# Kernel optimization log

Hardware: AMD Instinct MI355X
Metric: run time of the kernel (lower is better)

## Reference

```python
import jax, jax.numpy as jnp
import numpy as np

D = 256
NH = 8
HD = D // NH
B, HH, WW = 4, 28, 28
EPS = 1e-5

def _ln(x, g, b):
    m = jnp.mean(x, -1, keepdims=True)
    v = jnp.var(x, -1, keepdims=True)
    return (x - m) * jax.lax.rsqrt(v + EPS) * g + b

def _heads(x):
    b, n, _ = x.shape
    return x.reshape(b, n, NH, HD)

def _attn(q, k, v):
    # q,k,v: [B,N,D] -> multi-head SDPA, full NxN scores as in source
    qh, kh, vh = _heads(q), _heads(k), _heads(v)
    s = jnp.einsum('bqhd,bkhd->bhqk', qh, kh) * (HD ** -0.5)
    a = jax.nn.softmax(s, axis=-1)
    o = jnp.einsum('bhqk,bkhd->bqhd', a, vh)
    return o.reshape(q.shape)

def setup_inputs():
    key = jax.random.key(0)
    ks = iter(jax.random.split(key, 80))
    def rn(shape, s):
        return jax.random.normal(next(ks), shape, jnp.float32) * s
    w = D ** -0.5
    inp = {}
    for n in ('f1', 'f2', 'f3', 'f4'):
        inp[n] = rn((B, D, HH, WW), 1.0)
    for n in ('Wq_a', 'Wk_a', 'Wv_a', 'Wq_b', 'Wk_b', 'Wv_b'):
        inp[n] = rn((4, D, D), w)
    for n in ('bq_a', 'bk_a', 'bv_a', 'bq_b', 'bk_b', 'bv_b'):
        inp[n] = jnp.zeros((4, D), jnp.float32)
    inp['gamma'] = rn((4,), 0.5)
    inp['gamma_ffn'] = rn((4,), 0.5)
    inp['Wfuse'] = rn((4, 2 * D, D), w)
    inp['bfuse'] = jnp.zeros((4, D), jnp.float32)
    inp['W1'] = rn((4, D, 4 * D), w)
    inp['b1'] = jnp.zeros((4, 4 * D), jnp.float32)
    inp['W2'] = rn((4, 4 * D, D), (4 * D) ** -0.5)
    inp['b2'] = jnp.zeros((4, D), jnp.float32)
    inp['ln1_g'] = jnp.ones((4, D), jnp.float32)
    inp['ln1_b'] = jnp.zeros((4, D), jnp.float32)
    inp['ln2_g'] = jnp.ones((4, D), jnp.float32)
    inp['ln2_b'] = jnp.zeros((4, D), jnp.float32)
    inp['fp_ln_g'] = jnp.ones((D,), jnp.float32)
    inp['fp_ln_b'] = jnp.zeros((D,), jnp.float32)
    inp['fp_W'] = rn((D, D), w)
    inp['fp_b'] = jnp.zeros((D,), jnp.float32)
    inp['ff_ln_g'] = jnp.ones((4 * D,), jnp.float32)
    inp['ff_ln_b'] = jnp.zeros((4 * D,), jnp.float32)
    inp['ff_W'] = rn((4 * D, D), (4 * D) ** -0.5)
    inp['ff_b'] = jnp.zeros((D,), jnp.float32)
    inp['mha_Wqkv'] = rn((D, 3 * D), w)
    inp['mha_bqkv'] = jnp.zeros((3 * D,), jnp.float32)
    inp['mha_Wo'] = rn((D, D), w)
    inp['mha_bo'] = jnp.zeros((D,), jnp.float32)
    inp['norm_g'] = jnp.ones((D,), jnp.float32)
    inp['norm_b'] = jnp.zeros((D,), jnp.float32)
    return inp

def reference(f1, f2, f3, f4, Wq_a, Wk_a, Wv_a, Wq_b, Wk_b, Wv_b,
              bq_a, bk_a, bv_a, bq_b, bk_b, bv_b, gamma, gamma_ffn,
              Wfuse, bfuse, W1, b1, W2, b2, ln1_g, ln1_b, ln2_g, ln2_b,
              fp_ln_g, fp_ln_b, fp_W, fp_b, ff_ln_g, ff_ln_b, ff_W, ff_b,
              mha_Wqkv, mha_bqkv, mha_Wo, mha_bo, norm_g, norm_b):
    to_seq = lambda x: x.transpose(0, 2, 3, 1).reshape(x.shape[0], -1, x.shape[1])

    def block(i, xa, xb):
        # BiDirectionalCrossAttention.forward (dropout inactive in eval)
        qa = xa @ Wq_a[i] + bq_a[i]
        kb = xb @ Wk_b[i] + bk_b[i]
        vb = xb @ Wv_b[i] + bv_b[i]
        qb = xb @ Wq_b[i] + bq_b[i]
        ka = xa @ Wk_a[i] + bk_a[i]
        va = xa @ Wv_a[i] + bv_a[i]
        a2b = _attn(qa, kb, vb)
        b2a = _attn(qb, ka, va)
        fused = jnp.concatenate([a2b, b2a], -1) @ Wfuse[i] + bfuse[i]
        xa1 = _ln(xa + jnp.tanh(gamma[i]) * fused, ln1_g[i], ln1_b[i])
        ffn = jax.nn.gelu(xa1 @ W1[i] + b1[i], approximate=False) @ W2[i] + b2[i]
        return _ln(xa1 + jnp.tanh(gamma_ffn[i]) * ffn, ln2_g[i], ln2_b[i])

    s1, s2, s3, s4 = to_seq(f1), to_seq(f2), to_seq(f3), to_seq(f4)
    # block indices: 0=cross_attn_1_2, 1=cross_attn_1_4, 2=cross_attn_2_3, 3=cross_attn_3_4
    e1 = (block(0, s1, s2) + block(1, s1, s4)) / 2
    e2 = (block(0, s2, s1) + block(2, s2, s3)) / 2
    e3 = (block(2, s3, s2) + block(3, s3, s4)) / 2
    e4 = (block(1, s4, s1) + block(3, s4, s3)) / 2
    fp = lambda x: jax.nn.gelu(_ln(x, fp_ln_g, fp_ln_b) @ fp_W + fp_b, approximate=False)
    allf = jnp.concatenate([fp(e1), fp(e2), fp(e3), fp(e4)], -1)
    x = jax.nn.gelu(_ln(allf, ff_ln_g, ff_ln_b) @ ff_W + ff_b, approximate=False)
    # nn.MultiheadAttention self-attention (no residual in source)
    qkv = x @ mha_Wqkv + mha_bqkv
    q, k, v = jnp.split(qkv, 3, axis=-1)
    attn_out = _attn(q, k, v) @ mha_Wo + mha_bo
    x = _ln(attn_out, norm_g, norm_b)
    return x.reshape(B, HH, WW, D).transpose(0, 3, 1, 2)
```

## Files before the change

### kernel.cpp

```cpp
#include <hip/hip_runtime.h>

typedef unsigned short u16;
typedef __bf16 bf16x8 __attribute__((ext_vector_type(8)));
typedef float f32x4 __attribute__((ext_vector_type(4)));
typedef float f32x16 __attribute__((ext_vector_type(16)));
typedef unsigned short u16x8 __attribute__((ext_vector_type(8)));
typedef unsigned short u16x4 __attribute__((ext_vector_type(4)));

static constexpr size_t MD = 802816;

__device__ __forceinline__ u16 f2bf(float f) {
    __bf16 h = (__bf16)f;
    return __builtin_bit_cast(unsigned short, h);
}
__device__ __forceinline__ float bf2f(u16 u) {
    return __uint_as_float(((unsigned)u) << 16);
}
__device__ __forceinline__ float gelu_f(float x) {
    return 0.5f * x * (1.0f + erff(x * 0.70710678118654752f));
}
__device__ __forceinline__ unsigned cvt_pk_bf16(float a, float b) {
    unsigned r;
    asm("v_cvt_pk_bf16_f32 %0, %1, %2" : "=v"(r) : "v"(a), "v"(b));
    return r;
}
__device__ __forceinline__ float exp2_hw(float x) {
    float r;
    asm("v_exp_f32 %0, %1" : "=v"(r) : "v"(x));
    return r;
}
__device__ __forceinline__ int xcd_swz(int id, int nwg) {
    int q = nwg >> 3, r = nwg & 7;
    int xcd = id & 7, idx = id >> 3;
    return (xcd < r) ? (xcd * (q + 1) + idx) : (r * (q + 1) + (xcd - r) * q + idx);
}
union u8_4 { u16x8 v8; u16x4 v4[2]; };
union bf8_4 { bf16x8 f; u16x4 h[2]; u16x8 v8; };

__device__ __forceinline__ void gemm_core(
    const u16* __restrict__ A, int lda,
    const u16* __restrict__ Bt, int K,
    const float* __restrict__ bias,
    u16* __restrict__ C, int ldc, int act, int m0, int n0,
    u16* __restrict__ VT)
{
    __shared__ u16 As[64][72];
    __shared__ u16 Bs[64][72];
    const int tid  = threadIdx.x;
    const int wave = tid >> 6, lane = tid & 63;
    const int wr = wave >> 1, wc = wave & 1;
    const int l16 = lane & 15, kg = lane >> 4, kb = kg * 8;
    const int srow = tid >> 2, scol = (tid & 3) * 16;

    f32x4 acc[2][2];
#pragma unroll
    for (int j = 0; j < 2; j++)
#pragma unroll
        for (int i = 0; i < 2; i++) { f32x4 z = {0.f,0.f,0.f,0.f}; acc[j][i] = z; }

    const u16* ap = A + (size_t)(m0 + srow) * lda + scol;
    const u16* bp = Bt + (size_t)(n0 + srow) * K + scol;
    u16x8 ua0 = *(const u16x8*)ap;
    u16x8 ua1 = *(const u16x8*)(ap + 8);
    u16x8 ub0 = *(const u16x8*)bp;
    u16x8 ub1 = *(const u16x8*)(bp + 8);

    for (int kt = 0; kt < K; kt += 64) {
        *(u16x8*)&As[srow][scol]     = ua0;
        *(u16x8*)&As[srow][scol + 8] = ua1;
        *(u16x8*)&Bs[srow][scol]     = ub0;
        *(u16x8*)&Bs[srow][scol + 8] = ub1;
        __syncthreads();
        if (kt + 64 < K) {
            ua0 = *(const u16x8*)(ap + kt + 64);
            ua1 = *(const u16x8*)(ap + kt + 72);
            ub0 = *(const u16x8*)(bp + kt + 64);
            ub1 = *(const u16x8*)(bp + kt + 72);
        }
#pragma unroll
        for (int h = 0; h < 2; h++) {
            bf16x8 af[2], bf[2];
#pragma unroll
            for (int j = 0; j < 2; j++)
                af[j] = *(const bf16x8*)&Bs[wc*32 + j*16 + l16][h*32 + kb];
#pragma unroll
            for (int i = 0; i < 2; i++)
                bf[i] = *(const bf16x8*)&As[wr*32 + i*16 + l16][h*32 + kb];
#pragma unroll
            for (int j = 0; j < 2; j++)
#pragma unroll
                for (int i = 0; i < 2; i++)
                    acc[j][i] = __builtin_amdgcn_mfma_f32_16x16x32_bf16(
                        af[j], bf[i], acc[j][i], 0,0,0);
        }
        __syncthreads();
    }
#pragma unroll
    for (int j = 0; j < 2; j++) {
        int lcol = wc*32 + j*16 + kg*4;
        f32x4 bv = *(const f32x4*)&bias[n0 + lcol];
#pragma unroll
        for (int i = 0; i < 2; i++) {
            int lrow = wr*32 + i*16 + l16;
            u16x4 o;
#pragma unroll
            for (int r = 0; r < 4; r++) {
                float v = acc[j][i][r] + bv[r];
                if (act == 1) v = gelu_f(v);
                o[r] = f2bf(v);
            }
            *(u16x4*)&As[lrow][lcol] = o;
        }
    }
    __syncthreads();
    if (VT && n0 >= 512) {
        int c = tid & 63, chunk = tid >> 6;
        int dg = n0 - 512 + c;
        int hh2 = dg >> 5, dd = dg & 31;
        int grow = m0 + chunk*16;
        int bb2 = grow / 784, kk0 = grow - bb2 * 784;
        u16x8 a, b;
#pragma unroll
        for (int j = 0; j < 8; j++) a[j] = As[chunk*16 + j][c];
#pragma unroll
        for (int j = 0; j < 8; j++) b[j] = As[chunk*16 + 8 + j][c];
        u16* vp = VT + ((size_t)(bb2*8 + hh2)*32 + dd)*784 + kk0;
        *(u16x8*)vp = a;
        *(u16x8*)(vp + 8) = b;
    } else {
        int crow = tid >> 2, cc = (tid & 3) * 16;
        u16x8 c0 = *(const u16x8*)&As[crow][cc];
        u16x8 c1 = *(const u16x8*)&As[crow][cc + 8];
        u16* cp = &C[(size_t)(m0 + crow) * ldc + n0 + cc];
        *(u16x8*)cp = c0;
        *(u16x8*)(cp + 8) = c1;
    }
}

__global__ __launch_bounds__(256) void gemm2_kernel(
    const u16* __restrict__ A, int lda, int zA,
    const u16* __restrict__ Bt, int K, int i0, int i1, int i2, int i3, int Bsz,
    const float* __restrict__ bias, int bN,
    u16* __restrict__ C, int ldc, int zC, int act, int nN, int nwg)
{
    int wg = xcd_swz(blockIdx.x, nwg);
    int n = wg % nN, rest = wg / nN;
    int m = rest % 49, z = rest / 49;
    int iz = (z == 0) ? i0 : (z == 1) ? i1 : (z == 2) ? i2 : i3;
    gemm_core(A + (size_t)z * zA, lda,
              Bt + (size_t)iz * Bsz, K,
              bias + (size_t)iz * bN,
              C + (size_t)z * zC, ldc, act, m * 64, n * 64, nullptr);
}

__global__ __launch_bounds__(256) void proj8_kernel(
    const u16* __restrict__ s, int b0, int b1, int b2, int b3,
    int i0, int i1, int i2, int i3,
    const u16* __restrict__ projWt, const float* __restrict__ biasc,
    u16* __restrict__ projc, u16* __restrict__ vt)
{
    int wg = xcd_swz(blockIdx.x, 4704);
    int n = wg % 12, rest = wg / 12;
    int m = rest % 49, z = rest / 49;
    int inv = z >> 1, ab = z & 1;
    int bi = (inv == 0) ? b0 : (inv == 1) ? b1 : (inv == 2) ? b2 : b3;
    int ii = (inv == 0) ? i0 : (inv == 1) ? i1 : (inv == 2) ? i2 : i3;
    const u16* Aact = s + (size_t)(ab ? bi : inv) * MD;
    int widx = ii * 2 + ab;
    gemm_core(Aact, 256, projWt + (size_t)widx * 768 * 256, 256,
              biasc + widx * 768,
              projc + (size_t)z * 3 * MD, 768, 0, m * 64, n * 64,
              vt + (size_t)(z ^ 1) * MD);
}

__global__ __launch_bounds__(256) void pack_bias_kernel(
    const float* b0, const float* b1, const float* b2,
    const float* b3, const float* b4, const float* b5,
    float* __restrict__ biasc)
{
    int z = blockIdx.x;
    int tsr = z >> 2, i = z & 3;
    const float* barr[6] = {b0,b1,b2,b3,b4,b5};
    int ab = (tsr >= 3) ? 1 : 0;
    biasc[(i*2 + ab)*768 + (tsr % 3)*256 + threadIdx.x] = barr[tsr][i*256 + threadIdx.x];
}

__device__ __forceinline__ void attn3_core(
    const u16* __restrict__ Qg, int ldq,
    const u16* __restrict__ Kg, int ldk,
    const u16* __restrict__ Vtg,
    u16* __restrict__ Og, int ldo,
    int qt, int rowbase, int qkcol, int ocol)
{
    __shared__ u16 Ks[2][64][36];
    __shared__ u16 Vts[2][32][68];
    __shared__ u16 Ps[4][32][68];
    __shared__ float Ls[4][32];

    const int tid = threadIdx.x, wave = tid >> 6, lane = tid & 63;
    const int l32 = lane & 31, hi = lane >> 5;
    const int sr = tid >> 2, sc8 = (tid & 3) * 8;
    const int vd = tid >> 3, vk8 = (tid & 7) * 8;
    const float QSC = 0.25503489f;

    bf8_4 qf0, qf1;
    {
        int qrow = qt*128 + wave*32 + l32;
        u16x8 z8 = {0,0,0,0,0,0,0,0};
        u16x8 q0 = z8, q1 = z8;
        if (qrow < 784) {
            const u16* qp = Qg + (size_t)(rowbase + qrow) * ldq + qkcol;
            q0 = *(const u16x8*)(qp + hi*8);
            q1 = *(const u16x8*)(qp + 16 + hi*8);
        }
#pragma unroll
        for (int j = 0; j < 8; j++) {
            q0[j] = f2bf(bf2f(q0[j]) * QSC);
            q1[j] = f2bf(bf2f(q1[j]) * QSC);
        }
        qf0.v8 = q0;
        qf1.v8 = q1;
    }
    {
        u8_4 k, v;
        k.v8 = *(const u16x8*)(Kg + (size_t)(rowbase + sr) * ldk + qkcol + sc8);
        v.v8 = *(const u16x8*)(Vtg + (size_t)vd * 784 + vk8);
        *(u16x4*)&Ks[0][sr][sc8]     = k.v4[0];
        *(u16x4*)&Ks[0][sr][sc8 + 4] = k.v4[1];
        *(u16x4*)&Vts[0][vd][vk8]     = v.v4[0];
        *(u16x4*)&Vts[0][vd][vk8 + 4] = v.v4[1];
    }
    __syncthreads();

    f32x16 oacc;
#pragma unroll
    for (int i = 0; i < 16; i++) oacc[i] = 0.f;
    float lsum = 0.f;

    u16x8 kr, vr;
    for (int t = 0; t < 13; ++t) {
        const int cur = t & 1;
        if (t < 12) {
            u16x8 z8 = {0,0,0,0,0,0,0,0}; kr = z8; vr = z8;
            int krow = (t+1)*64 + sr;
            if (krow < 784)
                kr = *(const u16x8*)(Kg + (size_t)(rowbase + krow) * ldk + qkcol + sc8);
            int kc = (t+1)*64 + vk8;
            if (kc + 7 < 784)
                vr = *(const u16x8*)(Vtg + (size_t)vd * 784 + kc);
        }
        const int kvalid = (t == 12) ? 16 : 64;
#pragma unroll
        for (int kb2 = 0; kb2 < 2; kb2++) {
            f32x16 sacc;
#pragma unroll
            for (int i = 0; i < 16; i++) sacc[i] = 0.f;
            bf8_4 kf0, kf1;
            kf0.h[0] = *(const u16x4*)&Ks[cur][kb2*32 + l32][hi*8];
            kf0.h[1] = *(const u16x4*)&Ks[cur][kb2*32 + l32][hi*8 + 4];
            kf1.h[0] = *(const u16x4*)&Ks[cur][kb2*32 + l32][16 + hi*8];
            kf1.h[1] = *(const u16x4*)&Ks[cur][kb2*32 + l32][16 + hi*8 + 4];
            sacc = __builtin_amdgcn_mfma_f32_32x32x16_bf16(kf0.f, qf0.f, sacc, 0,0,0);
            sacc = __builtin_amdgcn_mfma_f32_32x32x16_bf16(kf1.f, qf1.f, sacc, 0,0,0);
#pragma unroll
            for (int g = 0; g < 4; g++) {
                int k0 = kb2*32 + 8*g + 4*hi;
                union { unsigned u[2]; u16x4 v; } pk;
                if (k0 < kvalid) {
                    float p0 = exp2_hw(sacc[4*g+0]);
                    float p1 = exp2_hw(sacc[4*g+1]);
                    float p2 = exp2_hw(sacc[4*g+2]);
                    float p3 = exp2_hw(sacc[4*g+3]);
                    lsum += (p0 + p1) + (p2 + p3);
                    pk.u[0] = cvt_pk_bf16(p0, p1);
                    pk.u[1] = cvt_pk_bf16(p2, p3);
                } else { pk.u[0] = 0; pk.u[1] = 0; }
                *(u16x4*)&Ps[wave][l32][k0] = pk.v;
            }
        }
#pragma unroll
        for (int kf2 = 0; kf2 < 4; kf2++) {
            bf8_4 pf, vf;
            pf.h[0] = *(const u16x4*)&Ps[wave][l32][kf2*16 + hi*8];
            pf.h[1] = *(const u16x4*)&Ps[wave][l32][kf2*16 + hi*8 + 4];
            vf.h[0] = *(const u16x4*)&Vts[cur][l32][kf2*16 + hi*8];
            vf.h[1] = *(const u16x4*)&Vts[cur][l32][kf2*16 + hi*8 + 4];
            oacc = __builtin_amdgcn_mfma_f32_32x32x16_bf16(pf.f, vf.f, oacc, 0,0,0);
        }
        if (t < 12) {
            u8_4 k, v; k.v8 = kr; v.v8 = vr;
            *(u16x4*)&Ks[cur^1][sr][sc8]     = k.v4[0];
            *(u16x4*)&Ks[cur^1][sr][sc8 + 4] = k.v4[1];
            *(u16x4*)&Vts[cur^1][vd][vk8]     = v.v4[0];
            *(u16x4*)&Vts[cur^1][vd][vk8 + 4] = v.v4[1];
            __syncthreads();
        }
    }
    float lt = lsum + __shfl_xor(lsum, 32);
    if (hi == 0) Ls[wave][l32] = lt;
    f32x4 lv[4];
#pragma unroll
    for (int g = 0; g < 4; g++) lv[g] = *(const f32x4*)&Ls[wave][8*g + 4*hi];
#pragma unroll
    for (int g = 0; g < 4; g++)
#pragma unroll
        for (int j = 0; j < 4; j++) {
            int row = qt*128 + wave*32 + 8*g + 4*hi + j;
            if (row < 784)
                Og[(size_t)(rowbase + row) * ldo + ocol + l32] =
                    f2bf(oacc[4*g+j] * __builtin_amdgcn_rcpf(lv[g][j]));
        }
}

__global__ __launch_bounds__(256) void attn_pair_kernel(
    const u16* __restrict__ projc, const u16* __restrict__ vt,
    u16* __restrict__ fusedin)
{
    int id = blockIdx.x;
    int wg = (id & 7) * 224 + (id >> 3);
    int qt = wg % 7, bh = (wg / 7) & 31, z = wg / 224;
    int inv = z >> 1, dir = z & 1;
    const u16* Q  = projc + (size_t)z * 3 * MD;
    const u16* K  = projc + (size_t)(z ^ 1) * 3 * MD + 256;
    const u16* Vt = vt + (size_t)z * MD + (size_t)bh * 32 * 784;
    u16* O = fusedin + (size_t)inv * 2 * MD;
    int bb = bh >> 3, hh = bh & 7;
    attn3_core(Q, 768, K, 768, Vt, O, 512, qt, bb*784, hh*32, dir*256 + hh*32);
}

__global__ __launch_bounds__(256) void attn_mha_kernel(
    const u16* __restrict__ qkv, const u16* __restrict__ vtmha,
    u16* __restrict__ outp)
{
    int id = blockIdx.x;
    int wg = (id & 7) * 28 + (id >> 3);
    int qt = wg % 7, bh = wg / 7;
    int bb = bh >> 3, hh = bh & 7;
    const u16* Vt = vtmha + (size_t)bh * 32 * 784;
    attn3_core(qkv, 768, qkv + 256, 768, Vt, outp, 256, qt, bb*784, hh*32, hh*32);
}

__global__ __launch_bounds__(256) void ln_kernel(
    const u16* __restrict__ x, int zx,
    const u16* __restrict__ res, int zres,
    const float* __restrict__ gamma, int i0, int i1, int i2, int i3,
    const float* __restrict__ g, const float* __restrict__ beta, int gN,
    u16* __restrict__ out, int zout,
    float outscale, int accum, int D)
{
    int z = blockIdx.y;
    int iz = (z == 0) ? i0 : (z == 1) ? i1 : (z == 2) ? i2 : i3;
    const u16* xb = x + (size_t)z * zx;
    const u16* rb = res ? res + (size_t)z * zres : (const u16*)nullptr;
    u16* ob = out + (size_t)z * zout;
    const float* gg = g + iz * gN;
    const float* bb = beta + iz * gN;
    int wave = threadIdx.x >> 6, lane = threadIdx.x & 63;
    int half = lane >> 5, l32 = lane & 31;
    size_t row = (size_t)blockIdx.x * 8 + wave * 2 + half;
    float tg = gamma ? tanhf(gamma[iz]) : 1.0f;
    const u16* xr = xb + row * D;
    const u16* rr = rb ? rb + row * D : (const u16*)nullptr;
    float vals[32];
    int nch = D >> 8;
    float s = 0.f, s2 = 0.f;
    for (int c = 0; c < nch; c++) {
        int col = c * 256 + l32 * 8;
        u16x8 v = *(const u16x8*)(xr + col);
        u16x8 r8 = {0,0,0,0,0,0,0,0};
        if (rr) r8 = *(const u16x8*)(rr + col);
#pragma unroll
        for (int j = 0; j < 8; j++) {
            float a = tg * bf2f(v[j]) + bf2f(r8[j]);
            vals[c*8 + j] = a;
            s += a; s2 += a * a;
        }
    }
#pragma unroll
    for (int off = 1; off < 32; off <<= 1) {
        s  += __shfl_xor(s, off);
        s2 += __shfl_xor(s2, off);
    }
    float inv = 1.0f / D;
    float mean = s * inv;
    float var = s2 * inv - mean * mean;
    float rstd = rsqrtf(var + 1e-5f);
    for (int c = 0; c < nch; c++) {
        int col = c * 256 + l32 * 8;
        u16x8 prev = {0,0,0,0,0,0,0,0};
        if (accum) prev = *(const u16x8*)(ob + row*D + col);
        u16x8 o8;
#pragma unroll
        for (int j = 0; j < 8; j++) {
            float o = (vals[c*8 + j] - mean) * rstd * gg[col + j] + bb[col + j];
            o *= outscale;
            if (accum) o += bf2f(prev[j]);
            o8[j] = f2bf(o);
        }
        *(u16x8*)(ob + row*D + col) = o8;
    }
}

__device__ __forceinline__ void transpose_body(const float* in, u16* out, int K, int N)
{
    __shared__ float t[32][33];
    int tx = threadIdx.x, ty = threadIdx.y;
#pragma unroll
    for (int j = 0; j < 4; j++)
        t[ty + j*8][tx] = in[(size_t)(blockIdx.y*32 + ty + j*8) * N + blockIdx.x*32 + tx];
    __syncthreads();
#pragma unroll
    for (int j = 0; j < 4; j++)
        out[(size_t)(blockIdx.x*32 + ty + j*8) * K + blockIdx.y*32 + tx] =
            f2bf(t[tx][ty + j*8]);
}

__global__ __launch_bounds__(256) void transpose_w(const float* __restrict__ in,
                                                   u16* __restrict__ out, int K, int N)
{
    int z = blockIdx.z;
    transpose_body(in + (size_t)z * K * N, out + (size_t)z * K * N, K, N);
}

__global__ __launch_bounds__(256) void transpose_w6(
    const float* w0, const float* w1, const float* w2,
    const float* w3, const float* w4, const float* w5,
    u16* __restrict__ out)
{
    int z = blockIdx.z;
    int tsr = z >> 2, i = z & 3;
    const float* ws[6] = {w0,w1,w2,w3,w4,w5};
    int ab = (tsr >= 3) ? 1 : 0;
    u16* ob = out + (size_t)((i*2 + ab)*3 + (tsr % 3)) * 65536;
    transpose_body(ws[tsr] + (size_t)i * 65536, ob, 256, 256);
}

__global__ __launch_bounds__(256) void vtrans_kernel(
    const u16* __restrict__ base,
    u16* __restrict__ out)
{
    __shared__ u16 t[64][44];
    const u16* in = base + 512;
    int kt = blockIdx.x, bh = blockIdx.y;
    int bb = bh >> 3, hh = bh & 7;
    int tid = threadIdx.x;
    {
        int r = tid >> 2, c8 = (tid & 3) * 8;
        int krow = kt*64 + r;
        u16x8 u = {0,0,0,0,0,0,0,0};
        if (krow < 784)
            u = *(const u16x8*)(in + (size_t)(bb*784 + krow) * 768 + hh*32 + c8);
        *(u16x8*)&t[r][c8] = u;
    }
    __syncthreads();
    int d = tid >> 3, k8 = (tid & 7) * 8;
    if (kt*64 + k8 + 7 < 784) {
        u16x8 u;
#pragma unroll
        for (int j = 0; j < 8; j++) u[j] = t[k8 + j][d];
        *(u16x8*)&out[(size_t)(bh*32 + d) * 784 + kt*64 + k8] = u;
    }
}

__global__ __launch_bounds__(256) void to_seq_kernel(
    const float* f0, const float* f1, const float* f2, const float* f3,
    u16* __restrict__ sbase)
{
    __shared__ float t[16][17];
    int z = blockIdx.z;
    int fi = z & 3, b = z >> 2;
    const float* fs[4] = {f0,f1,f2,f3};
    const float* f = fs[fi] + (size_t)b * 256 * 784;
    u16* s = sbase + (size_t)fi * MD + (size_t)b * 784 * 256;
    int tx = threadIdx.x, ty = threadIdx.y;
    t[ty][tx] = f[(size_t)(blockIdx.y*16 + ty) * 784 + blockIdx.x*16 + tx];
    __syncthreads();
    s[(size_t)(blockIdx.x*16 + ty) * 256 + blockIdx.y*16 + tx] = f2bf(t[tx][ty]);
}

__global__ __launch_bounds__(256) void from_seq_kernel(const u16* __restrict__ y,
                                                       float* __restrict__ out)
{
    __shared__ float t[16][17];
    int b = blockIdx.z;
    const u16* yb = y + (size_t)b * 784 * 256;
    float* ob = out + (size_t)b * 256 * 784;
    int tx = threadIdx.x, ty = threadIdx.y;
    t[ty][tx] = bf2f(yb[(size_t)(blockIdx.x*16 + ty) * 256 + blockIdx.y*16 + tx]);
    __syncthreads();
    ob[(size_t)(blockIdx.y*16 + ty) * 784 + blockIdx.x*16 + tx] = t[tx][ty];
}

extern "C" void kernel_launch(void* const* d_in, const int* in_sizes, int n_in,
                              void* d_out, int out_size, void* d_ws, size_t ws_size,
                              hipStream_t stream)
{
    (void)in_sizes; (void)n_in; (void)out_size; (void)ws_size;
    const float* f0 = (const float*)d_in[0];
    const float* f1 = (const float*)d_in[1];
    const float* f2 = (const float*)d_in[2];
    const float* f3 = (const float*)d_in[3];
    const float* Wq_a = (const float*)d_in[4];
    const float* Wk_a = (const float*)d_in[5];
    const float* Wv_a = (const float*)d_in[6];
    const float* Wq_b = (const float*)d_in[7];
    const float* Wk_b = (const float*)d_in[8];
    const float* Wv_b = (const float*)d_in[9];
    const float* bq_a = (const float*)d_in[10];
    const float* bk_a = (const float*)d_in[11];
    const float* bv_a = (const float*)d_in[12];
    const float* bq_b = (const float*)d_in[13];
    const float* bk_b = (const float*)d_in[14];
    const float* bv_b = (const float*)d_in[15];
    const float* gamma = (const float*)d_in[16];
    const float* gamma_ffn = (const float*)d_in[17];
    const float* Wfuse = (const float*)d_in[18];
    const float* bfuse = (const float*)d_in[19];
    const float* W1 = (const float*)d_in[20];
    const float* b1 = (const float*)d_in[21];
    const float* W2 = (const float*)d_in[22];
    const float* b2 = (const float*)d_in[23];
    const float* ln1_g = (const float*)d_in[24];
    const float* ln1_b = (const float*)d_in[25];
    const float* ln2_g = (const float*)d_in[26];
    const float* ln2_b = (const float*)d_in[27];
    const float* fp_ln_g = (const float*)d_in[28];
    const float* fp_ln_b = (const float*)d_in[29];
    const float* fp_W = (const float*)d_in[30];
    const float* fp_b = (const float*)d_in[31];
    const float* ff_ln_g = (const float*)d_in[32];
    const float* ff_ln_b = (const float*)d_in[33];
    const float* ff_W = (const float*)d_in[34];
    const float* ff_b = (const float*)d_in[35];
    const float* mha_Wqkv = (const float*)d_in[36];
    const float* mha_bqkv = (const float*)d_in[37];
    const float* mha_Wo = (const float*)d_in[38];
    const float* mha_bo = (const float*)d_in[39];
    const float* norm_g = (const float*)d_in[40];
    const float* norm_b = (const float*)d_in[41];

    u16* W = (u16*)d_ws;
    u16* projWt = W;
    u16* fuseWt = projWt + 1572864;
    u16* W1t    = fuseWt + 524288;
    u16* W2t    = W1t + 1048576;
    u16* fpWt   = W2t + 1048576;
    u16* ffWt   = fpWt + 65536;
    u16* qkvWt  = ffWt + 262144;
    u16* WoWt   = qkvWt + 196608;
    float* biasc = (float*)(WoWt + 65536);
    u16* act    = (u16*)(biasc + 6144);

    u16* s     = act;
    u16* e     = act + 4*MD;
    u16* projc = act + 8*MD;
    u16* vt    = act + 32*MD;
    u16* fin   = act + 40*MD;
    u16* ffh  = projc;
    u16* fb   = projc + 16*MD;
    u16* xa1  = projc + 20*MD;
    u16* ffb  = vt;

    to_seq_kernel<<<dim3(49,16,16), dim3(16,16), 0, stream>>>(f0,f1,f2,f3, s);
    transpose_w6<<<dim3(8,8,24), dim3(32,8), 0, stream>>>(Wq_a,Wk_a,Wv_a,Wq_b,Wk_b,Wv_b, projWt);
    pack_bias_kernel<<<24, 256, 0, stream>>>(bq_a,bk_a,bv_a,bq_b,bk_b,bv_b, biasc);
    transpose_w<<<dim3(8,16,4), dim3(32,8), 0, stream>>>(Wfuse, fuseWt, 512, 256);
    transpose_w<<<dim3(32,8,4), dim3(32,8), 0, stream>>>(W1, W1t, 256, 1024);
    transpose_w<<<dim3(8,32,4), dim3(32,8), 0, stream>>>(W2, W2t, 1024, 256);
    transpose_w<<<dim3(8,8,1),  dim3(32,8), 0, stream>>>(fp_W, fpWt, 256, 256);
    transpose_w<<<dim3(8,32,1), dim3(32,8), 0, stream>>>(ff_W, ffWt, 1024, 256);
    transpose_w<<<dim3(24,8,1), dim3(32,8), 0, stream>>>(mha_Wqkv, qkvWt, 256, 768);
    transpose_w<<<dim3(8,8,1),  dim3(32,8), 0, stream>>>(mha_Wo, WoWt, 256, 256);

    const int GI[2][4] = {{0,0,2,1},{1,2,3,3}};
    const int GB[2][4] = {{1,0,1,0},{3,2,3,2}};

    for (int g = 0; g < 2; g++) {
        int i0 = GI[g][0], i1 = GI[g][1], i2 = GI[g][2], i3 = GI[g][3];
        proj8_kernel<<<4704, 256, 0, stream>>>(s,
            GB[g][0], GB[g][1], GB[g][2], GB[g][3], i0, i1, i2, i3,
            projWt, biasc, projc, vt);
        attn_pair_kernel<<<1792, 256, 0, stream>>>(projc, vt, fin);
        gemm2_kernel<<<784, 256, 0, stream>>>(fin, 512, (int)(2*MD),
            fuseWt, 512, i0, i1, i2, i3, 131072, bfuse, 256, fb, 256, (int)MD, 0, 4, 784);
        ln_kernel<<<dim3(392,4), 256, 0, stream>>>(fb, (int)MD,
            s, (int)MD, gamma, i0, i1, i2, i3, ln1_g, ln1_b, 256,
            xa1, (int)MD, 1.0f, 0, 256);
        gemm2_kernel<<<3136, 256, 0, stream>>>(xa1, 256, (int)MD,
            W1t, 256, i0, i1, i2, i3, 262144, b1, 1024, ffh, 1024, (int)(4*MD), 1, 16, 3136);
        gemm2_kernel<<<784, 256, 0, stream>>>(ffh, 1024, (int)(4*MD),
            W2t, 1024, i0, i1, i2, i3, 262144, b2, 256, ffb, 256, (int)MD, 0, 4, 784);
        ln_kernel<<<dim3(392,4), 256, 0, stream>>>(ffb, (int)MD,
            xa1, (int)MD, gamma_ffn, i0, i1, i2, i3, ln2_g, ln2_b, 256,
            e, (int)MD, 0.5f, g, 256);
    }

    u16* ln4    = act + 8*MD;
    u16* allf   = act + 12*MD;
    u16* ffln   = act + 16*MD;
    u16* x2     = act + 20*MD;
    u16* qkv    = act + 21*MD;
    u16* vtmha  = act + 24*MD;
    u16* attn_o = act + 25*MD;
    u16* ymid   = act + 26*MD;
    u16* yfin   = act + 27*MD;

    ln_kernel<<<dim3(392,4), 256, 0, stream>>>(e, (int)MD,
        (const u16*)nullptr, 0, (const float*)nullptr, 0,0,0,0,
        fp_ln_g, fp_ln_b, 0, ln4, (int)MD, 1.0f, 0, 256);
    gemm2_kernel<<<784, 256, 0, stream>>>(ln4, 256, (int)MD,
        fpWt, 256, 0,0,0,0, 0, fp_b, 0, allf, 1024, 256, 1, 4, 784);
    ln_kernel<<<dim3(392,1), 256, 0, stream>>>(allf, 0,
        (const u16*)nullptr, 0, (const float*)nullptr, 0,0,0,0,
        ff_ln_g, ff_ln_b, 0, ffln, 0, 1.0f, 0, 1024);
    gemm2_kernel<<<196, 256, 0, stream>>>(ffln, 1024, 0,
        ffWt, 1024, 0,0,0,0, 0, ff_b, 0, x2, 256, 0, 1, 4, 196);
    gemm2_kernel<<<588, 256, 0, stream>>>(x2, 256, 0,
        qkvWt, 256, 0,0,0,0, 0, mha_bqkv, 0, qkv, 768, 0, 0, 12, 588);
    vtrans_kernel<<<dim3(13,32), 256, 0, stream>>>(qkv, vtmha);
    attn_mha_kernel<<<224, 256, 0, stream>>>(qkv, vtmha, attn_o);
    gemm2_kernel<<<196, 256, 0, stream>>>(attn_o, 256, 0,
        WoWt, 256, 0,0,0,0, 0, mha_bo, 0, ymid, 256, 0, 0, 4, 196);
    ln_kernel<<<dim3(392,1), 256, 0, stream>>>(ymid, 0,
        (const u16*)nullptr, 0, (const float*)nullptr, 0,0,0,0,
        norm_g, norm_b, 0, yfin, 0, 1.0f, 0, 256);
    from_seq_kernel<<<dim3(49,16,4), dim3(16,16), 0, stream>>>(yfin, (float*)d_out);
}
```

Baseline: 366.1 us.

## Merge both block groups into single wide launches and batch weight transposes

When the workspace is large enough, the two sequential groups of four cross-attention blocks run as one set of launches over all eight blocks, doubling grid sizes and halving launch count. The Q/K projection buffer drops the unused V columns (stride 512 instead of 768). The seven weight transpose launches are merged into one kernel driven by a descriptor table. The accumulate-in-LN averaging is replaced by writing both block outputs separately and summing them in the next LN via the residual path. This costs more workspace memory and adds a fallback path when the workspace is too small.

```diff
diff --git a/kernel.cpp b/kernel.cpp
--- a/kernel.cpp
+++ b/kernel.cpp
@@ -139,37 +139,37 @@
 
 __global__ __launch_bounds__(256) void gemm2_kernel(
     const u16* __restrict__ A, int lda, int zA,
-    const u16* __restrict__ Bt, int K, int i0, int i1, int i2, int i3, int Bsz,
+    const u16* __restrict__ Bt, int K, int ipack, int Bsz,
     const float* __restrict__ bias, int bN,
     u16* __restrict__ C, int ldc, int zC, int act, int nN, int nwg)
 {
     int wg = xcd_swz(blockIdx.x, nwg);
     int n = wg % nN, rest = wg / nN;
     int m = rest % 49, z = rest / 49;
-    int iz = (z == 0) ? i0 : (z == 1) ? i1 : (z == 2) ? i2 : i3;
+    int iz = (ipack >> (2*z)) & 3;
     gemm_core(A + (size_t)z * zA, lda,
               Bt + (size_t)iz * Bsz, K,
               bias + (size_t)iz * bN,
               C + (size_t)z * zC, ldc, act, m * 64, n * 64, nullptr);
 }
 
-__global__ __launch_bounds__(256) void proj8_kernel(
-    const u16* __restrict__ s, int b0, int b1, int b2, int b3,
-    int i0, int i1, int i2, int i3,
+__global__ __launch_bounds__(256) void proj_kernel(
+    const u16* __restrict__ s, int apack, int bpack, int ipack,
     const u16* __restrict__ projWt, const float* __restrict__ biasc,
-    u16* __restrict__ projc, u16* __restrict__ vt)
-{
-    int wg = xcd_swz(blockIdx.x, 4704);
+    u16* __restrict__ projqk, u16* __restrict__ vt, int nwg)
+{
+    int wg = xcd_swz(blockIdx.x, nwg);
     int n = wg % 12, rest = wg / 12;
     int m = rest % 49, z = rest / 49;
     int inv = z >> 1, ab = z & 1;
-    int bi = (inv == 0) ? b0 : (inv == 1) ? b1 : (inv == 2) ? b2 : b3;
-    int ii = (inv == 0) ? i0 : (inv == 1) ? i1 : (inv == 2) ? i2 : i3;
-    const u16* Aact = s + (size_t)(ab ? bi : inv) * MD;
+    int ai = (apack >> (2*inv)) & 3;
+    int bi = (bpack >> (2*inv)) & 3;
+    int ii = (ipack >> (2*inv)) & 3;
+    const u16* Aact = s + (size_t)(ab ? bi : ai) * MD;
     int widx = ii * 2 + ab;
     gemm_core(Aact, 256, projWt + (size_t)widx * 768 * 256, 256,
               biasc + widx * 768,
-              projc + (size_t)z * 3 * MD, 768, 0, m * 64, n * 64,
+              projqk + (size_t)z * 2 * MD, 512, 0, m * 64, n * 64,
               vt + (size_t)(z ^ 1) * MD);
 }
 
@@ -313,19 +313,20 @@
 }
 
 __global__ __launch_bounds__(256) void attn_pair_kernel(
-    const u16* __restrict__ projc, const u16* __restrict__ vt,
-    u16* __restrict__ fusedin)
+    const u16* __restrict__ projqk, const u16* __restrict__ vt,
+    u16* __restrict__ fin)
 {
     int id = blockIdx.x;
-    int wg = (id & 7) * 224 + (id >> 3);
+    int nper = gridDim.x >> 3;
+    int wg = (id & 7) * nper + (id >> 3);
     int qt = wg % 7, bh = (wg / 7) & 31, z = wg / 224;
     int inv = z >> 1, dir = z & 1;
-    const u16* Q  = projc + (size_t)z * 3 * MD;
-    const u16* K  = projc + (size_t)(z ^ 1) * 3 * MD + 256;
+    const u16* Q  = projqk + (size_t)z * 2 * MD;
+    const u16* K  = projqk + (size_t)(z ^ 1) * 2 * MD + 256;
     const u16* Vt = vt + (size_t)z * MD + (size_t)bh * 32 * 784;
-    u16* O = fusedin + (size_t)inv * 2 * MD;
+    u16* O = fin + (size_t)inv * 2 * MD;
     int bb = bh >> 3, hh = bh & 7;
-    attn3_core(Q, 768, K, 768, Vt, O, 512, qt, bb*784, hh*32, dir*256 + hh*32);
+    attn3_core(Q, 512, K, 512, Vt, O, 512, qt, bb*784, hh*32, dir*256 + hh*32);
 }
 
 __global__ __launch_bounds__(256) void attn_mha_kernel(
@@ -341,24 +342,25 @@
 }
 
 __global__ __launch_bounds__(256) void ln_kernel(
-    const u16* __restrict__ x, int zx,
-    const u16* __restrict__ res, int zres,
-    const float* __restrict__ gamma, int i0, int i1, int i2, int i3,
+    const u16* __restrict__ x, size_t zx,
+    const u16* __restrict__ res, size_t zres, int respack,
+    const float* __restrict__ gamma, int gpack,
     const float* __restrict__ g, const float* __restrict__ beta, int gN,
-    u16* __restrict__ out, int zout,
-    float outscale, int accum, int D)
+    u16* __restrict__ out, size_t zout,
+    float outscale, int D)
 {
     int z = blockIdx.y;
-    int iz = (z == 0) ? i0 : (z == 1) ? i1 : (z == 2) ? i2 : i3;
+    int gi = (gpack >> (2*z)) & 3;
     const u16* xb = x + (size_t)z * zx;
-    const u16* rb = res ? res + (size_t)z * zres : (const u16*)nullptr;
+    const u16* rb = res ? res + (size_t)z * zres + (size_t)((respack >> (2*z)) & 3) * MD
+                        : (const u16*)nullptr;
     u16* ob = out + (size_t)z * zout;
-    const float* gg = g + iz * gN;
-    const float* bb = beta + iz * gN;
+    const float* gg = g + gi * gN;
+    const float* bb = beta + gi * gN;
     int wave = threadIdx.x >> 6, lane = threadIdx.x & 63;
     int half = lane >> 5, l32 = lane & 31;
     size_t row = (size_t)blockIdx.x * 8 + wave * 2 + half;
-    float tg = gamma ? tanhf(gamma[iz]) : 1.0f;
+    float tg = gamma ? tanhf(gamma[gi]) : 1.0f;
     const u16* xr = xb + row * D;
     const u16* rr = rb ? rb + row * D : (const u16*)nullptr;
     float vals[32];
@@ -387,39 +389,47 @@
     float rstd = rsqrtf(var + 1e-5f);
     for (int c = 0; c < nch; c++) {
         int col = c * 256 + l32 * 8;
-        u16x8 prev = {0,0,0,0,0,0,0,0};
-        if (accum) prev = *(const u16x8*)(ob + row*D + col);
         u16x8 o8;
 #pragma unroll
         for (int j = 0; j < 8; j++) {
             float o = (vals[c*8 + j] - mean) * rstd * gg[col + j] + bb[col + j];
-            o *= outscale;
-            if (accum) o += bf2f(prev[j]);
-            o8[j] = f2bf(o);
+            o8[j] = f2bf(o * outscale);
         }
         *(u16x8*)(ob + row*D + col) = o8;
     }
 }
 
-__device__ __forceinline__ void transpose_body(const float* in, u16* out, int K, int N)
+__device__ __forceinline__ void transpose_body(const float* in, u16* out,
+                                               int K, int N, int bx, int by)
 {
     __shared__ float t[32][33];
     int tx = threadIdx.x, ty = threadIdx.y;
 #pragma unroll
     for (int j = 0; j < 4; j++)
-        t[ty + j*8][tx] = in[(size_t)(blockIdx.y*32 + ty + j*8) * N + blockIdx.x*32 + tx];
+        t[ty + j*8][tx] = in[(size_t)(by*32 + ty + j*8) * N + bx*32 + tx];
     __syncthreads();
 #pragma unroll
     for (int j = 0; j < 4; j++)
-        out[(size_t)(blockIdx.x*32 + ty + j*8) * K + blockIdx.y*32 + tx] =
+        out[(size_t)(bx*32 + ty + j*8) * K + by*32 + tx] =
             f2bf(t[tx][ty + j*8]);
 }
 
-__global__ __launch_bounds__(256) void transpose_w(const float* __restrict__ in,
-                                                   u16* __restrict__ out, int K, int N)
-{
-    int z = blockIdx.z;
-    transpose_body(in + (size_t)z * K * N, out + (size_t)z * K * N, K, N);
+struct TDesc { const float* in; u16* out; int K, N, start, bpz; };
+struct TPack7 { TDesc d[7]; };
+
+__global__ __launch_bounds__(256) void tmerge_kernel(TPack7 p)
+{
+    int bid = blockIdx.x;
+    int di = 0;
+#pragma unroll
+    for (int i = 1; i < 7; i++) if (bid >= p.d[i].start) di = i;
+    TDesc d = p.d[di];
+    int local = bid - d.start;
+    int zz = local / d.bpz, rem = local - zz * d.bpz;
+    int nbx = d.N >> 5;
+    int bx = rem % nbx, by = rem / nbx;
+    transpose_body(d.in + (size_t)zz * d.K * d.N,
+                   d.out + (size_t)zz * d.K * d.N, d.K, d.N, bx, by);
 }
 
 __global__ __launch_bounds__(256) void transpose_w6(
@@ -432,7 +442,8 @@
     const float* ws[6] = {w0,w1,w2,w3,w4,w5};
     int ab = (tsr >= 3) ? 1 : 0;
     u16* ob = out + (size_t)((i*2 + ab)*3 + (tsr % 3)) * 65536;
-    transpose_body(ws[tsr] + (size_t)i * 65536, ob, 256, 256);
+    transpose_body(ws[tsr] + (size_t)i * 65536, ob, 256, 256,
+                   blockIdx.x, blockIdx.y);
 }
 
 __global__ __launch_bounds__(256) void vtrans_kernel(
@@ -495,7 +506,7 @@
                               void* d_out, int out_size, void* d_ws, size_t ws_size,
                               hipStream_t stream)
 {
-    (void)in_sizes; (void)n_in; (void)out_size; (void)ws_size;
+    (void)in_sizes; (void)n_in; (void)out_size;
     const float* f0 = (const float*)d_in[0];
     const float* f1 = (const float*)d_in[1];
     const float* f2 = (const float*)d_in[2];
@@ -551,78 +562,121 @@
     float* biasc = (float*)(WoWt + 65536);
     u16* act    = (u16*)(biasc + 6144);
 
-    u16* s     = act;
-    u16* e     = act + 4*MD;
-    u16* projc = act + 8*MD;
-    u16* vt    = act + 32*MD;
-    u16* fin   = act + 40*MD;
-    u16* ffh  = projc;
-    u16* fb   = projc + 16*MD;
-    u16* xa1  = projc + 20*MD;
-    u16* ffb  = vt;
+    u16* s    = act;
+    u16* e8   = act + 4*MD;
+    u16* main_ = act + 12*MD;
+
+    const size_t actbytes_merged = (size_t)2 * 76 * MD;
+    const size_t weights_bytes = (size_t)((char*)act - (char*)d_ws);
+    const bool merged = ws_size >= weights_bytes + actbytes_merged;
 
     to_seq_kernel<<<dim3(49,16,16), dim3(16,16), 0, stream>>>(f0,f1,f2,f3, s);
     transpose_w6<<<dim3(8,8,24), dim3(32,8), 0, stream>>>(Wq_a,Wk_a,Wv_a,Wq_b,Wk_b,Wv_b, projWt);
     pack_bias_kernel<<<24, 256, 0, stream>>>(bq_a,bk_a,bv_a,bq_b,bk_b,bv_b, biasc);
-    transpose_w<<<dim3(8,16,4), dim3(32,8), 0, stream>>>(Wfuse, fuseWt, 512, 256);
-    transpose_w<<<dim3(32,8,4), dim3(32,8), 0, stream>>>(W1, W1t, 256, 1024);
-    transpose_w<<<dim3(8,32,4), dim3(32,8), 0, stream>>>(W2, W2t, 1024, 256);
-    transpose_w<<<dim3(8,8,1),  dim3(32,8), 0, stream>>>(fp_W, fpWt, 256, 256);
-    transpose_w<<<dim3(8,32,1), dim3(32,8), 0, stream>>>(ff_W, ffWt, 1024, 256);
-    transpose_w<<<dim3(24,8,1), dim3(32,8), 0, stream>>>(mha_Wqkv, qkvWt, 256, 768);
-    transpose_w<<<dim3(8,8,1),  dim3(32,8), 0, stream>>>(mha_Wo, WoWt, 256, 256);
-
-    const int GI[2][4] = {{0,0,2,1},{1,2,3,3}};
-    const int GB[2][4] = {{1,0,1,0},{3,2,3,2}};
-
-    for (int g = 0; g < 2; g++) {
-        int i0 = GI[g][0], i1 = GI[g][1], i2 = GI[g][2], i3 = GI[g][3];
-        proj8_kernel<<<4704, 256, 0, stream>>>(s,
-            GB[g][0], GB[g][1], GB[g][2], GB[g][3], i0, i1, i2, i3,
-            projWt, biasc, projc, vt);
-        attn_pair_kernel<<<1792, 256, 0, stream>>>(projc, vt, fin);
-        gemm2_kernel<<<784, 256, 0, stream>>>(fin, 512, (int)(2*MD),
-            fuseWt, 512, i0, i1, i2, i3, 131072, bfuse, 256, fb, 256, (int)MD, 0, 4, 784);
-        ln_kernel<<<dim3(392,4), 256, 0, stream>>>(fb, (int)MD,
-            s, (int)MD, gamma, i0, i1, i2, i3, ln1_g, ln1_b, 256,
-            xa1, (int)MD, 1.0f, 0, 256);
-        gemm2_kernel<<<3136, 256, 0, stream>>>(xa1, 256, (int)MD,
-            W1t, 256, i0, i1, i2, i3, 262144, b1, 1024, ffh, 1024, (int)(4*MD), 1, 16, 3136);
-        gemm2_kernel<<<784, 256, 0, stream>>>(ffh, 1024, (int)(4*MD),
-            W2t, 1024, i0, i1, i2, i3, 262144, b2, 256, ffb, 256, (int)MD, 0, 4, 784);
-        ln_kernel<<<dim3(392,4), 256, 0, stream>>>(ffb, (int)MD,
-            xa1, (int)MD, gamma_ffn, i0, i1, i2, i3, ln2_g, ln2_b, 256,
-            e, (int)MD, 0.5f, g, 256);
-    }
-
-    u16* ln4    = act + 8*MD;
-    u16* allf   = act + 12*MD;
-    u16* ffln   = act + 16*MD;
-    u16* x2     = act + 20*MD;
-    u16* qkv    = act + 21*MD;
-    u16* vtmha  = act + 24*MD;
-    u16* attn_o = act + 25*MD;
-    u16* ymid   = act + 26*MD;
-    u16* yfin   = act + 27*MD;
-
-    ln_kernel<<<dim3(392,4), 256, 0, stream>>>(e, (int)MD,
-        (const u16*)nullptr, 0, (const float*)nullptr, 0,0,0,0,
-        fp_ln_g, fp_ln_b, 0, ln4, (int)MD, 1.0f, 0, 256);
+    {
+        TPack7 tp;
+        tp.d[0] = { Wfuse,    fuseWt, 512, 256,    0, 128 };
+        tp.d[1] = { W1,       W1t,    256, 1024, 512, 256 };
+        tp.d[2] = { W2,       W2t,   1024, 256, 1536, 256 };
+        tp.d[3] = { fp_W,     fpWt,   256, 256, 2560,  64 };
+        tp.d[4] = { ff_W,     ffWt,  1024, 256, 2624, 256 };
+        tp.d[5] = { mha_Wqkv, qkvWt,  256, 768, 2880, 192 };
+        tp.d[6] = { mha_Wo,   WoWt,   256, 256, 3072,  64 };
+        tmerge_kernel<<<3136, dim3(32,8), 0, stream>>>(tp);
+    }
+
+    const int IA[8] = {0,1,0,2,2,3,1,3};
+    const int AA[8] = {0,0,1,1,2,2,3,3};
+    const int BB[8] = {1,3,0,2,1,3,0,2};
+
+    if (merged) {
+        u16* projqk = main_;
+        u16* vt  = main_ + 32*MD;
+        u16* fin = main_ + 48*MD;
+        u16* ffh = projqk;
+        u16* fb  = vt;
+        u16* xa1 = vt + 8*MD;
+        u16* ffb = fin;
+        int ip = 0, apk = 0, bpk = 0;
+        for (int j = 0; j < 8; j++) {
+            ip  |= IA[j] << (2*j);
+            apk |= AA[j] << (2*j);
+            bpk |= BB[j] << (2*j);
+        }
+        proj_kernel<<<9408, 256, 0, stream>>>(s, apk, bpk, ip,
+            projWt, biasc, projqk, vt, 9408);
+        attn_pair_kernel<<<3584, 256, 0, stream>>>(projqk, vt, fin);
+        gemm2_kernel<<<1568, 256, 0, stream>>>(fin, 512, (int)(2*MD),
+            fuseWt, 512, ip, 131072, bfuse, 256, fb, 256, (int)MD, 0, 4, 1568);
+        ln_kernel<<<dim3(392,8), 256, 0, stream>>>(fb, MD,
+            s, 0, apk, gamma, ip, ln1_g, ln1_b, 256, xa1, MD, 1.0f, 256);
+        gemm2_kernel<<<6272, 256, 0, stream>>>(xa1, 256, (int)MD,
+            W1t, 256, ip, 262144, b1, 1024, ffh, 1024, (int)(4*MD), 1, 16, 6272);
+        gemm2_kernel<<<1568, 256, 0, stream>>>(ffh, 1024, (int)(4*MD),
+            W2t, 1024, ip, 262144, b2, 256, ffb, 256, (int)MD, 0, 4, 1568);
+        ln_kernel<<<dim3(392,8), 256, 0, stream>>>(ffb, MD,
+            xa1, MD, 0, gamma_ffn, ip, ln2_g, ln2_b, 256, e8, MD, 0.5f, 256);
+    } else {
+        u16* projqk = main_;
+        u16* vt  = main_ + 16*MD;
+        u16* fin = main_ + 24*MD;
+        u16* ffh = projqk;
+        u16* fb  = vt;
+        u16* xa1 = vt + 4*MD;
+        u16* ffb = fin;
+        for (int g = 0; g < 2; g++) {
+            int ip = 0, apk = 0, bpk = 0;
+            for (int j = 0; j < 4; j++) {
+                int bi = 2*j + g;
+                ip  |= IA[bi] << (2*j);
+                apk |= AA[bi] << (2*j);
+                bpk |= BB[bi] << (2*j);
+            }
+            proj_kernel<<<4704, 256, 0, stream>>>(s, apk, bpk, ip,
+                projWt, biasc, projqk, vt, 4704);
+            attn_pair_kernel<<<1792, 256, 0, stream>>>(projqk, vt, fin);
+            gemm2_kernel<<<784, 256, 0, stream>>>(fin, 512, (int)(2*MD),
+                fuseWt, 512, ip, 131072, bfuse, 256, fb, 256, (int)MD, 0, 4, 784);
+            ln_kernel<<<dim3(392,4), 256, 0, stream>>>(fb, MD,
+                s, 0, apk, gamma, ip, ln1_g, ln1_b, 256, xa1, MD, 1.0f, 256);
+            gemm2_kernel<<<3136, 256, 0, stream>>>(xa1, 256, (int)MD,
+                W1t, 256, ip, 262144, b1, 1024, ffh, 1024, (int)(4*MD), 1, 16, 3136);
+            gemm2_kernel<<<784, 256, 0, stream>>>(ffh, 1024, (int)(4*MD),
+                W2t, 1024, ip, 262144, b2, 256, ffb, 256, (int)MD, 0, 4, 784);
+            ln_kernel<<<dim3(392,4), 256, 0, stream>>>(ffb, MD,
+                xa1, MD, 0, gamma_ffn, ip, ln2_g, ln2_b, 256,
+                e8 + (size_t)g*MD, 2*MD, 0.5f, 256);
+        }
+    }
+
+    u16* ln4    = main_;
+    u16* allf   = main_ + 4*MD;
+    u16* ffln   = main_ + 8*MD;
+    u16* x2     = main_ + 12*MD;
+    u16* qkv    = main_ + 13*MD;
+    u16* vtmha  = main_ + 16*MD;
+    u16* attn_o = main_ + 17*MD;
+    u16* ymid   = main_ + 18*MD;
+    u16* yfin   = main_ + 19*MD;
+
+    ln_kernel<<<dim3(392,4), 256, 0, stream>>>(e8, 2*MD,
+        e8 + MD, 2*MD, 0, (const float*)nullptr, 0,
+        fp_ln_g, fp_ln_b, 0, ln4, MD, 1.0f, 256);
     gemm2_kernel<<<784, 256, 0, stream>>>(ln4, 256, (int)MD,
-        fpWt, 256, 0,0,0,0, 0, fp_b, 0, allf, 1024, 256, 1, 4, 784);
+        fpWt, 256, 0, 0, fp_b, 0, allf, 1024, 256, 1, 4, 784);
     ln_kernel<<<dim3(392,1), 256, 0, stream>>>(allf, 0,
-        (const u16*)nullptr, 0, (const float*)nullptr, 0,0,0,0,
-        ff_ln_g, ff_ln_b, 0, ffln, 0, 1.0f, 0, 1024);
+        (const u16*)nullptr, 0, 0, (const float*)nullptr, 0,
+        ff_ln_g, ff_ln_b, 0, ffln, 0, 1.0f, 1024);
     gemm2_kernel<<<196, 256, 0, stream>>>(ffln, 1024, 0,
-        ffWt, 1024, 0,0,0,0, 0, ff_b, 0, x2, 256, 0, 1, 4, 196);
+        ffWt, 1024, 0, 0, ff_b, 0, x2, 256, 0, 1, 4, 196);
     gemm2_kernel<<<588, 256, 0, stream>>>(x2, 256, 0,
-        qkvWt, 256, 0,0,0,0, 0, mha_bqkv, 0, qkv, 768, 0, 0, 12, 588);
+        qkvWt, 256, 0, 0, mha_bqkv, 0, qkv, 768, 0, 0, 12, 588);
     vtrans_kernel<<<dim3(13,32), 256, 0, stream>>>(qkv, vtmha);
     attn_mha_kernel<<<224, 256, 0, stream>>>(qkv, vtmha, attn_o);
     gemm2_kernel<<<196, 256, 0, stream>>>(attn_o, 256, 0,
-        WoWt, 256, 0,0,0,0, 0, mha_bo, 0, ymid, 256, 0, 0, 4, 196);
+        WoWt, 256, 0, 0, mha_bo, 0, ymid, 256, 0, 0, 4, 196);
     ln_kernel<<<dim3(392,1), 256, 0, stream>>>(ymid, 0,
-        (const u16*)nullptr, 0, (const float*)nullptr, 0,0,0,0,
-        norm_g, norm_b, 0, yfin, 0, 1.0f, 0, 256);
+        (const u16*)nullptr, 0, 0, (const float*)nullptr, 0,
+        norm_g, norm_b, 0, yfin, 0, 1.0f, 256);
     from_seq_kernel<<<dim3(49,16,4), dim3(16,16), 0, stream>>>(yfin, (float*)d_out);
 }
```

Measured after the change: 314.8 us. -14.0%, faster.
